# Kernel tuning notes

Hardware: AMD Instinct MI355X
Metric: run time of the kernel (lower is better)

Reference implementation:

```python
import jax, jax.numpy as jnp
import numpy as np

N = 500_000   # points
K = 16        # top-level components
S = 2         # subcomponents per component
D = 32        # repr_dim
EPS = 1e-10


def setup_inputs() -> dict:
    key = jax.random.key(0)
    k1, k2, k3 = jax.random.split(key, 3)
    X = jax.random.normal(k1, (N, D), dtype=jnp.float32)
    # responsibilities are row-stochastic in the original EM loop
    r = jax.nn.softmax(jax.random.normal(k2, (N, K), dtype=jnp.float32), axis=-1)
    ri = jax.nn.softmax(jax.random.normal(k3, (N, K * S), dtype=jnp.float32), axis=-1)
    return {"X": X, "r": r, "ri": ri}


def _m_step(X, z, ri):
    """Fused segment-reduce M-step: equivalent to the per-cluster python loop
    X_k = X[z==i]; r_k = ri[z==i, S*i:S*(i+1)]; weighted mean/cov per subcomp,
    but computed in one pass via one-hot gating of the responsibilities."""
    n = X.shape[0]
    mask = jax.nn.one_hot(z, K, dtype=X.dtype)                 # [N, K]
    pi = ri.sum(axis=0) / n                                    # [K*S]
    # gate subcluster responsibilities by hard top-level assignment
    w = (ri.reshape(n, K, S) * mask[:, :, None]).reshape(n, K * S)  # [N, K*S]
    denom = w.sum(axis=0)                                      # [K*S]  (= r_k.sum(0) per cluster)
    safe = jnp.maximum(denom, EPS)
    mus = jnp.einsum('nk,nd->kd', w, X) / safe[:, None]        # [K*S, D]
    # weighted second moment per component; loop via lax.map over the small
    # fixed K*S axis to avoid an [N, K*S, D] intermediate
    def second_moment(wk):
        return (X * wk[:, None]).T @ X                         # [D, D]
    m2 = jax.lax.map(second_moment, w.T) / safe[:, None, None] # [K*S, D, D]
    covs = m2 - mus[:, :, None] * mus[:, None, :]              # E[xx^T] - mu mu^T
    return pi, mus, covs


def reference(X, r, ri):
    z = jnp.argmax(r, axis=-1)   # [N] hard top-level assignment
    return _m_step(X, z, ri)
```

## Files before the change

kernel.cpp:

```cpp
#include <hip/hip_runtime.h>

#define AS1 __attribute__((address_space(1)))
#define AS3 __attribute__((address_space(3)))
#define CHUNK 256
#define NB 256

typedef unsigned int uint;
typedef unsigned short ushort;
typedef __attribute__((ext_vector_type(4))) float f32x4;
typedef __attribute__((ext_vector_type(8))) _Float16 h8;
typedef __attribute__((ext_vector_type(2))) __fp16 fp16x2;

union H8 { uint u[4]; h8 h; };

__device__ __forceinline__ void gld_lds16(const float* g, float* l) {
  __builtin_amdgcn_global_load_lds((const AS1 void*)g, (AS3 void*)l, 16, 0, 0);
}
__device__ __forceinline__ uint pkrtz(float a, float b) {
  union { fp16x2 h; uint u; } c;
  c.h = __builtin_amdgcn_cvt_pkrtz(a, b);
  return c.u;
}

#define WAITVM0  do { asm volatile("s_waitcnt vmcnt(0)" ::: "memory"); __builtin_amdgcn_sched_barrier(0); } while (0)
#define WAITLGKM do { asm volatile("s_waitcnt lgkmcnt(0)" ::: "memory"); __builtin_amdgcn_sched_barrier(0); } while (0)
#define BAR __builtin_amdgcn_s_barrier()

#define CLUSTER_MFMA(CIDX, B, T00a,T01a,T11a,T20a,T21a, T00b,T01b,T11b,T20b,T21b) { \
  const int c_ = (CIDX); \
  int cnt_ = lcnt[B][c_]; if (cnt_ > 64) cnt_ = 64; \
  const int ng_ = (cnt_ + 31) >> 5; \
  for (int g_ = 0; g_ < ng_; ++g_) { \
    alignas(16) ushort praw_[8]; \
    *(uint4*)praw_ = *(const uint4*)&list[B][c_][(g_ << 5) + ((l >> 4) << 3)]; \
    const int sbase_ = (g_ << 5) + ((l >> 4) << 3); \
    int p_[8]; \
    _Pragma("unroll") for (int j = 0; j < 8; ++j) \
      p_[j] = (sbase_ + j < cnt_) ? (int)praw_[j] : 256; \
    uint W_[8]; \
    _Pragma("unroll") for (int j = 0; j < 8; ++j) W_[j] = wls[B][p_[j]]; \
    H8 F0_, F1_, ws0_, ws1_; \
    _Pragma("unroll") for (int j = 0; j < 4; ++j) { \
      uint l0 = xh[p_[2*j]*34 + c16], l1 = xh[p_[2*j+1]*34 + c16]; \
      uint h0 = xh[p_[2*j]*34 + 16 + c16], h1 = xh[p_[2*j+1]*34 + 16 + c16]; \
      F0_.u[j] = l0 | (l1 << 16); \
      F1_.u[j] = h0 | (h1 << 16); \
      ws0_.u[j] = (W_[2*j] & 0xffffu) | (W_[2*j+1] << 16); \
      ws1_.u[j] = (W_[2*j] >> 16) | (W_[2*j+1] & 0xffff0000u); \
    } \
    H8 s00_, s01_, s10_, s11_, i20_, i21_; \
    s00_.h = F0_.h * ws0_.h; s01_.h = F1_.h * ws0_.h; \
    s10_.h = F0_.h * ws1_.h; s11_.h = F1_.h * ws1_.h; \
    _Pragma("unroll") for (int j = 0; j < 4; ++j) { \
      i20_.u[j] = lane16 ? ws0_.u[j] : 0u; \
      i21_.u[j] = lane16 ? ws1_.u[j] : 0u; \
    } \
    T00a = __builtin_amdgcn_mfma_f32_16x16x32_f16(s00_.h, s00_.h, T00a, 0,0,0); \
    T01a = __builtin_amdgcn_mfma_f32_16x16x32_f16(s00_.h, s01_.h, T01a, 0,0,0); \
    T11a = __builtin_amdgcn_mfma_f32_16x16x32_f16(s01_.h, s01_.h, T11a, 0,0,0); \
    T20a = __builtin_amdgcn_mfma_f32_16x16x32_f16(i20_.h, s00_.h, T20a, 0,0,0); \
    T21a = __builtin_amdgcn_mfma_f32_16x16x32_f16(i20_.h, s01_.h, T21a, 0,0,0); \
    T00b = __builtin_amdgcn_mfma_f32_16x16x32_f16(s10_.h, s10_.h, T00b, 0,0,0); \
    T01b = __builtin_amdgcn_mfma_f32_16x16x32_f16(s10_.h, s11_.h, T01b, 0,0,0); \
    T11b = __builtin_amdgcn_mfma_f32_16x16x32_f16(s11_.h, s11_.h, T11b, 0,0,0); \
    T20b = __builtin_amdgcn_mfma_f32_16x16x32_f16(i21_.h, s10_.h, T20b, 0,0,0); \
    T21b = __builtin_amdgcn_mfma_f32_16x16x32_f16(i21_.h, s11_.h, T21b, 0,0,0); \
  } }

#define STORE_MFMA(COMP, T00,T01,T11,T20,T21) { \
  float* dst_ = m2p + ((size_t)blockIdx.x * 32 + (COMP)) * 768; \
  const int r0_ = (l >> 4) << 2; \
  f32x4 t00_ = T00, t01_ = T01, t11_ = T11; \
  *(float4*)&dst_[c16 * 16 + r0_] = *(float4*)&t00_; \
  *(float4*)&dst_[256 + c16 * 16 + r0_] = *(float4*)&t11_; \
  *(float4*)&dst_[512 + c16 * 16 + r0_] = *(float4*)&t01_; \
  if (l < 16) { \
    musp[((size_t)blockIdx.x * 32 + (COMP)) * 32 + l] = T20[0]; \
    musp[((size_t)blockIdx.x * 32 + (COMP)) * 32 + 16 + l] = T21[0]; \
  } }

__global__ __launch_bounds__(512, 1) void giant_k(
    const float* __restrict__ X, const float* __restrict__ r,
    const float* __restrict__ ri,
    float* __restrict__ m2p, float* __restrict__ musp, float* __restrict__ dnp,
    float* __restrict__ pigp, int n, int nchunks)
{
  __shared__ float xf32[CHUNK * 32];
  __shared__ float ril[CHUNK * 32];
  __shared__ __align__(16) ushort xh[257 * 34];
  __shared__ uint wls[2][257];
  __shared__ __align__(16) ushort list[2][16][64];
  __shared__ int lcnt[2][16];
  __shared__ float dn[16][2];

  const int t = threadIdx.x;
  const int wv = t >> 6;
  const int l = t & 63;
  const int c16 = l & 15;
  const bool lane16 = (l & 15) == 0;
  const int G = gridDim.x;

  f32x4 z4 = {0.f, 0.f, 0.f, 0.f};
  f32x4 a0_00=z4, a0_01=z4, a0_11=z4, a0_20=z4, a0_21=z4;
  f32x4 b0_00=z4, b0_01=z4, b0_11=z4, b0_20=z4, b0_21=z4;
  f32x4 a1_00=z4, a1_01=z4, a1_11=z4, a1_20=z4, a1_21=z4;
  f32x4 b1_00=z4, b1_01=z4, b1_11=z4, b1_20=z4, b1_21=z4;
  float4 ppi = make_float4(0.f, 0.f, 0.f, 0.f);
  float4 rA = ppi, rB = ppi, rC = ppi, rD = ppi;

  auto STAGEX = [&](int ch) {
#pragma unroll
    for (int q = 0; q < 4; ++q) {
      int gi = ch * CHUNK + wv * 32 + q * 8 + (l >> 3);
      if (gi > n - 1) gi = n - 1;
      gld_lds16(X + (size_t)gi * 32 + ((l & 7) << 2), &xf32[(wv * 32 + q * 8) * 32]);
    }
  };
  auto STAGERI = [&](int ch) {
#pragma unroll
    for (int q = 0; q < 4; ++q) {
      int gi = ch * CHUNK + wv * 32 + q * 8 + (l >> 3);
      if (gi > n - 1) gi = n - 1;
      gld_lds16(ri + (size_t)gi * 32 + ((l & 7) << 2), &ril[(wv * 32 + q * 8) * 32]);
    }
  };
  auto LOADR = [&](int ch) {
    if (t < CHUNK) {
      int gi = ch * CHUNK + t;
      if (gi > n - 1) gi = n - 1;
      const float4* rr = (const float4*)(r + (size_t)gi * 16);
      rA = rr[0]; rB = rr[1]; rC = rr[2]; rD = rr[3];
    }
  };
  auto PREP = [&](int ch, int b) {
    int rem = n - ch * CHUNK; if (rem > CHUNK) rem = CHUNK;
    {
      const int p = t >> 1, hh = t & 1;
      const float4* s4c = (const float4*)(xf32 + p * 32 + hh * 16);
      uint* dst = (uint*)&xh[p * 34 + hh * 16];
#pragma unroll
      for (int i = 0; i < 4; ++i) {
        int ii = (i + p) & 3;
        float4 v = s4c[ii];
        dst[2 * ii]     = pkrtz(v.x, v.y);
        dst[2 * ii + 1] = pkrtz(v.z, v.w);
      }
    }
    if (t < rem) {
      float best = rA.x; int z = 0;
#define CHK(v, c) if ((v) > best) { best = (v); z = (c); }
      CHK(rA.y,1) CHK(rA.z,2) CHK(rA.w,3)
      CHK(rB.x,4) CHK(rB.y,5) CHK(rB.z,6) CHK(rB.w,7)
      CHK(rC.x,8) CHK(rC.y,9) CHK(rC.z,10) CHK(rC.w,11)
      CHK(rD.x,12) CHK(rD.y,13) CHK(rD.z,14) CHK(rD.w,15)
#undef CHK
      float2 w2 = *(const float2*)&ril[t * 32 + 2 * z];
      wls[b][t] = pkrtz(sqrtf(w2.x), sqrtf(w2.y));
      atomicAdd(&dn[z][0], w2.x);
      atomicAdd(&dn[z][1], w2.y);
      int pos = atomicAdd(&lcnt[b][z], 1);
      if (pos < 64) list[b][z][pos] = (ushort)t;
    }
    if (t < 16) lcnt[b ^ 1][t] = 0;
    const float4* r4 = (const float4*)ril;
#pragma unroll
    for (int k = 0; k < 4; ++k) {
      int fi = t + k * 512;
      if ((fi >> 3) < rem) {
        float4 v = r4[fi];
        ppi.x += v.x; ppi.y += v.y; ppi.z += v.z; ppi.w += v.w;
      }
    }
  };

  if (t < 32) { ((int*)lcnt)[t] = 0; ((float*)dn)[t] = 0.f; }
  if (t < 17) ((uint*)&xh[256 * 34])[t] = 0;
  if (t == 0) { wls[0][256] = 0; wls[1][256] = 0; }

  int ch = blockIdx.x;
  int b = 0;
  if (ch < nchunks) {
    STAGEX(ch); STAGERI(ch); LOADR(ch);
    WAITVM0; WAITLGKM; BAR;
    while (true) {
      PREP(ch, b);
      WAITLGKM; BAR;
      int chn = ch + G;
      if (chn < nchunks) { STAGEX(chn); STAGERI(chn); LOADR(chn); }
      CLUSTER_MFMA(wv * 2 + 0, b, a0_00,a0_01,a0_11,a0_20,a0_21,
                                  b0_00,b0_01,b0_11,b0_20,b0_21)
      CLUSTER_MFMA(wv * 2 + 1, b, a1_00,a1_01,a1_11,a1_20,a1_21,
                                  b1_00,b1_01,b1_11,b1_20,b1_21)
      if (chn >= nchunks) break;
      BAR;
      WAITVM0;
      b ^= 1; ch = chn;
    }
  }

  STORE_MFMA((wv * 2 + 0) * 2 + 0, a0_00,a0_01,a0_11,a0_20,a0_21)
  STORE_MFMA((wv * 2 + 0) * 2 + 1, b0_00,b0_01,b0_11,b0_20,b0_21)
  STORE_MFMA((wv * 2 + 1) * 2 + 0, a1_00,a1_01,a1_11,a1_20,a1_21)
  STORE_MFMA((wv * 2 + 1) * 2 + 1, b1_00,b1_01,b1_11,b1_20,b1_21)
  if (t < 32) dnp[blockIdx.x * 32 + t] = dn[t >> 1][t & 1];

  __syncthreads();
  float4* s4 = (float4*)ril;
  s4[t] = ppi;
  __syncthreads();
  if (t < 8) {
    float4 a = s4[t];
#pragma unroll
    for (int q = 1; q < 64; ++q) {
      float4 v = s4[t + q * 8];
      a.x += v.x; a.y += v.y; a.z += v.z; a.w += v.w;
    }
    *(float4*)&pigp[blockIdx.x * 32 + t * 4] = a;
  }
}

__global__ __launch_bounds__(256) void reduce_k(
    const float* __restrict__ m2p, const float* __restrict__ musp,
    const float* __restrict__ dnp, const float* __restrict__ pigp,
    float* __restrict__ m2r, float* __restrict__ musr,
    float* __restrict__ dnr, float* __restrict__ pigr8, int nb)
{
  const int t = threadIdx.x;
  const int bid = blockIdx.x;

  if (bid < 200) {
    __shared__ float4 red[256];
    const float* in; float* outp; int rs, colbase;
    if (bid < 192) { in = m2p;  outp = m2r;  rs = 24576; colbase = bid * 32; }
    else           { in = musp; outp = musr; rs = 1024;  colbase = (bid - 192) * 32; }
    const int col = colbase + (t & 31);
    float4 a = make_float4(0.f, 0.f, 0.f, 0.f);
#pragma unroll 4
    for (int bb = t >> 5; bb < nb; bb += 8) {
      float4 v = *(const float4*)&in[(size_t)bb * rs + col * 4];
      a.x += v.x; a.y += v.y; a.z += v.z; a.w += v.w;
    }
    red[t] = a;
    __syncthreads();
    if (t < 32) {
      float4 s = red[t];
#pragma unroll
      for (int q = 1; q < 8; ++q) {
        float4 v = red[t + q * 32];
        s.x += v.x; s.y += v.y; s.z += v.z; s.w += v.w;
      }
      *(float4*)&outp[col * 4] = s;
    }
  } else {
    __shared__ float redf[256];
    const float* in; float* outp; int rows, row0;
    if (bid == 200) { in = dnp; outp = dnr; rows = nb; row0 = 0; }
    else {
      in = pigp; outp = pigr8 + (bid - 201) * 32;
      rows = nb / 8; row0 = (bid - 201) * (nb / 8);
    }
    float a = 0.f;
    const int c = t & 31;
#pragma unroll 4
    for (int bb = t >> 5; bb < rows; bb += 8) a += in[(row0 + bb) * 32 + c];
    redf[t] = a;
    __syncthreads();
    if (t < 32) {
      float s = redf[t];
#pragma unroll
      for (int q = 1; q < 8; ++q) s += redf[t + q * 32];
      outp[c] = s;
    }
  }
}

__global__ __launch_bounds__(256) void finalize_k(
    const float* __restrict__ pigr8, const float* __restrict__ dnr,
    const float* __restrict__ musr, const float* __restrict__ m2r,
    float* __restrict__ out, int n)
{
  const int c = blockIdx.x;
  const int t = threadIdx.x;
  __shared__ float mu[32];
  float safe = fmaxf(dnr[c], 1e-10f);
  if (t < 32) {
    float m = musr[c * 32 + t] / safe;
    mu[t] = m;
    out[32 + c * 32 + t] = m;
  }
  if (c == 0 && t < 32) {
    float p = 0.f;
#pragma unroll
    for (int s = 0; s < 8; ++s) p += pigr8[s * 32 + t];
    out[t] = p / (float)n;
  }
  __syncthreads();
  const int d1 = t >> 3;
  const int c0 = (t * 4) & 31;
  const float* base = m2r + c * 768;
  float vals[4];
  if (d1 < 16) {
    if (c0 < 16) {
      float4 v = *(const float4*)&base[d1 * 16 + c0];
      vals[0]=v.x; vals[1]=v.y; vals[2]=v.z; vals[3]=v.w;
    } else {
      int cc = c0 - 16;
#pragma unroll
      for (int j = 0; j < 4; ++j) vals[j] = base[512 + (cc + j) * 16 + d1];
    }
  } else {
    int dd = d1 - 16;
    if (c0 < 16) {
      float4 v = *(const float4*)&base[512 + dd * 16 + c0];
      vals[0]=v.x; vals[1]=v.y; vals[2]=v.z; vals[3]=v.w;
    } else {
      float4 v = *(const float4*)&base[256 + dd * 16 + (c0 - 16)];
      vals[0]=v.x; vals[1]=v.y; vals[2]=v.z; vals[3]=v.w;
    }
  }
  float mud1 = mu[d1];
  float4 cov;
  cov.x = vals[0] / safe - mud1 * mu[c0 + 0];
  cov.y = vals[1] / safe - mud1 * mu[c0 + 1];
  cov.z = vals[2] / safe - mud1 * mu[c0 + 2];
  cov.w = vals[3] / safe - mud1 * mu[c0 + 3];
  *(float4*)&out[32 + 1024 + c * 1024 + t * 4] = cov;
}

extern "C" void kernel_launch(void* const* d_in, const int* in_sizes, int n_in,
                              void* d_out, int out_size, void* d_ws, size_t ws_size,
                              hipStream_t stream) {
  const float* X  = (const float*)d_in[0];
  const float* r  = (const float*)d_in[1];
  const float* ri = (const float*)d_in[2];
  float* out = (float*)d_out;
  const int n = in_sizes[0] / 32;
  const int nchunks = (n + CHUNK - 1) / CHUNK;

  float* m2p   = (float*)d_ws;
  float* musp  = m2p + (size_t)NB * 32 * 768;
  float* dnp   = musp + (size_t)NB * 32 * 32;
  float* m2r   = dnp + (size_t)NB * 32;
  float* musr  = m2r + 24576;
  float* dnr   = musr + 1024;
  float* pigr8 = dnr + 32;
  float* pigp  = pigr8 + 8 * 32;

  giant_k<<<NB, 512, 0, stream>>>(X, r, ri, m2p, musp, dnp, pigp, n, nchunks);
  reduce_k<<<209, 256, 0, stream>>>(m2p, musp, dnp, pigp, m2r, musr, dnr, pigr8, NB);
  finalize_k<<<32, 256, 0, stream>>>(pigr8, dnr, musr, m2r, out, n);
}
```

Measured before the change: 53.71 us.

## Drop LDS staging of ri and r, load directly in PREP for 2 blocks/CU

Removes the 32KB ril LDS buffer and the prefetched r registers. r and ri are now read straight from global memory inside PREP, and the pi partial sums accumulate from register loads. Launch bounds move to two blocks per CU so occupancy can rise. The cost is that the r/ri loads are no longer prefetched during the previous chunk's MFMA work, and PREP gets an extra barrier plus a dependent global gather of the gated ri pair.

```diff
diff --git a/kernel.cpp b/kernel.cpp
--- a/kernel.cpp
+++ b/kernel.cpp
@@ -79,25 +79,27 @@
     musp[((size_t)blockIdx.x * 32 + (COMP)) * 32 + 16 + l] = T21[0]; \
   } }
 
-__global__ __launch_bounds__(512, 1) void giant_k(
+__global__ __launch_bounds__(512, 2) void giant_k(
     const float* __restrict__ X, const float* __restrict__ r,
     const float* __restrict__ ri,
     float* __restrict__ m2p, float* __restrict__ musp, float* __restrict__ dnp,
     float* __restrict__ pigp, int n, int nchunks)
 {
   __shared__ float xf32[CHUNK * 32];
-  __shared__ float ril[CHUNK * 32];
   __shared__ __align__(16) ushort xh[257 * 34];
   __shared__ uint wls[2][257];
   __shared__ __align__(16) ushort list[2][16][64];
   __shared__ int lcnt[2][16];
   __shared__ float dn[16][2];
+  __shared__ unsigned char zs[256];
 
   const int t = threadIdx.x;
   const int wv = t >> 6;
   const int l = t & 63;
   const int c16 = l & 15;
   const bool lane16 = (l & 15) == 0;
+  const int cg = t & 7;
+  const int pr = t >> 3;
   const int G = gridDim.x;
 
   f32x4 z4 = {0.f, 0.f, 0.f, 0.f};
@@ -106,7 +108,7 @@
   f32x4 a1_00=z4, a1_01=z4, a1_11=z4, a1_20=z4, a1_21=z4;
   f32x4 b1_00=z4, b1_01=z4, b1_11=z4, b1_20=z4, b1_21=z4;
   float4 ppi = make_float4(0.f, 0.f, 0.f, 0.f);
-  float4 rA = ppi, rB = ppi, rC = ppi, rD = ppi;
+  const float4* rif = (const float4*)ri;
 
   auto STAGEX = [&](int ch) {
 #pragma unroll
@@ -116,24 +118,27 @@
       gld_lds16(X + (size_t)gi * 32 + ((l & 7) << 2), &xf32[(wv * 32 + q * 8) * 32]);
     }
   };
-  auto STAGERI = [&](int ch) {
-#pragma unroll
-    for (int q = 0; q < 4; ++q) {
-      int gi = ch * CHUNK + wv * 32 + q * 8 + (l >> 3);
-      if (gi > n - 1) gi = n - 1;
-      gld_lds16(ri + (size_t)gi * 32 + ((l & 7) << 2), &ril[(wv * 32 + q * 8) * 32]);
-    }
-  };
-  auto LOADR = [&](int ch) {
-    if (t < CHUNK) {
-      int gi = ch * CHUNK + t;
-      if (gi > n - 1) gi = n - 1;
+
+  auto PREP = [&](int ch, int b) {
+    int rem = n - ch * CHUNK; if (rem > CHUNK) rem = CHUNK;
+    const int base = ch * CHUNK;
+    float4 rA, rB, rC, rD;
+    {
+      int gi = base + (t & 255); if (gi > n - 1) gi = n - 1;
       const float4* rr = (const float4*)(r + (size_t)gi * 16);
       rA = rr[0]; rB = rr[1]; rC = rr[2]; rD = rr[3];
     }
-  };
-  auto PREP = [&](int ch, int b) {
-    int rem = n - ch * CHUNK; if (rem > CHUNK) rem = CHUNK;
+    float4 v0, v1, v2, v3;
+    {
+      int g0 = base + pr;        if (g0 > n - 1) g0 = n - 1;
+      int g1 = base + pr + 64;   if (g1 > n - 1) g1 = n - 1;
+      int g2 = base + pr + 128;  if (g2 > n - 1) g2 = n - 1;
+      int g3 = base + pr + 192;  if (g3 > n - 1) g3 = n - 1;
+      v0 = rif[(size_t)g0 * 8 + cg];
+      v1 = rif[(size_t)g1 * 8 + cg];
+      v2 = rif[(size_t)g2 * 8 + cg];
+      v3 = rif[(size_t)g3 * 8 + cg];
+    }
     {
       const int p = t >> 1, hh = t & 1;
       const float4* s4c = (const float4*)(xf32 + p * 32 + hh * 16);
@@ -146,6 +151,10 @@
         dst[2 * ii + 1] = pkrtz(v.z, v.w);
       }
     }
+    if (pr < rem)       { ppi.x += v0.x; ppi.y += v0.y; ppi.z += v0.z; ppi.w += v0.w; }
+    if (pr + 64 < rem)  { ppi.x += v1.x; ppi.y += v1.y; ppi.z += v1.z; ppi.w += v1.w; }
+    if (pr + 128 < rem) { ppi.x += v2.x; ppi.y += v2.y; ppi.z += v2.z; ppi.w += v2.w; }
+    if (pr + 192 < rem) { ppi.x += v3.x; ppi.y += v3.y; ppi.z += v3.z; ppi.w += v3.w; }
     if (t < rem) {
       float best = rA.x; int z = 0;
 #define CHK(v, c) if ((v) > best) { best = (v); z = (c); }
@@ -154,22 +163,18 @@
       CHK(rC.x,8) CHK(rC.y,9) CHK(rC.z,10) CHK(rC.w,11)
       CHK(rD.x,12) CHK(rD.y,13) CHK(rD.z,14) CHK(rD.w,15)
 #undef CHK
-      float2 w2 = *(const float2*)&ril[t * 32 + 2 * z];
+      zs[t] = (unsigned char)z;
+      int pos = atomicAdd(&lcnt[b][z], 1);
+      if (pos < 64) list[b][z][pos] = (ushort)t;
+    }
+    if (t < 16) lcnt[b ^ 1][t] = 0;
+    WAITLGKM; BAR;
+    if (t < rem) {
+      int z = zs[t];
+      float2 w2 = *(const float2*)(ri + (size_t)(base + t) * 32 + 2 * z);
       wls[b][t] = pkrtz(sqrtf(w2.x), sqrtf(w2.y));
       atomicAdd(&dn[z][0], w2.x);
       atomicAdd(&dn[z][1], w2.y);
-      int pos = atomicAdd(&lcnt[b][z], 1);
-      if (pos < 64) list[b][z][pos] = (ushort)t;
-    }
-    if (t < 16) lcnt[b ^ 1][t] = 0;
-    const float4* r4 = (const float4*)ril;
-#pragma unroll
-    for (int k = 0; k < 4; ++k) {
-      int fi = t + k * 512;
-      if ((fi >> 3) < rem) {
-        float4 v = r4[fi];
-        ppi.x += v.x; ppi.y += v.y; ppi.z += v.z; ppi.w += v.w;
-      }
     }
   };
 
@@ -180,13 +185,13 @@
   int ch = blockIdx.x;
   int b = 0;
   if (ch < nchunks) {
-    STAGEX(ch); STAGERI(ch); LOADR(ch);
+    STAGEX(ch);
     WAITVM0; WAITLGKM; BAR;
     while (true) {
       PREP(ch, b);
       WAITLGKM; BAR;
       int chn = ch + G;
-      if (chn < nchunks) { STAGEX(chn); STAGERI(chn); LOADR(chn); }
+      if (chn < nchunks) STAGEX(chn);
       CLUSTER_MFMA(wv * 2 + 0, b, a0_00,a0_01,a0_11,a0_20,a0_21,
                                   b0_00,b0_01,b0_11,b0_20,b0_21)
       CLUSTER_MFMA(wv * 2 + 1, b, a1_00,a1_01,a1_11,a1_20,a1_21,
@@ -205,7 +210,7 @@
   if (t < 32) dnp[blockIdx.x * 32 + t] = dn[t >> 1][t & 1];
 
   __syncthreads();
-  float4* s4 = (float4*)ril;
+  float4* s4 = (float4*)xf32;
   s4[t] = ppi;
   __syncthreads();
   if (t < 8) {
```

Result: slower. 55.76 us (+3.8%).
